# Optimization experiments

Hardware: AMD Instinct MI355X
Metric: run time of the kernel (lower is better)

The kernel has to match this reference:

```python
import jax, jax.numpy as jnp
import numpy as np

IN_C = 256
KEY_C = 256
VAL_C = 256
HEADS = 8


def setup_inputs() -> dict:
    key = jax.random.key(0)
    ks = jax.random.split(key, 9)
    s = 0.02
    return {
        "x": jax.random.normal(ks[0], (4, 8192, IN_C), dtype=jnp.float32),
        "Wk": jax.random.normal(ks[1], (KEY_C, IN_C), dtype=jnp.float32) * s,
        "bk": jax.random.normal(ks[2], (KEY_C,), dtype=jnp.float32) * s,
        "Wq": jax.random.normal(ks[3], (KEY_C, IN_C), dtype=jnp.float32) * s,
        "bq": jax.random.normal(ks[4], (KEY_C,), dtype=jnp.float32) * s,
        "Wv": jax.random.normal(ks[5], (VAL_C, IN_C), dtype=jnp.float32) * s,
        "bv": jax.random.normal(ks[6], (VAL_C,), dtype=jnp.float32) * s,
        "Wr": jax.random.normal(ks[7], (IN_C, VAL_C), dtype=jnp.float32) * s,
        "br": jax.random.normal(ks[8], (IN_C,), dtype=jnp.float32) * s,
    }


def reference(x, Wk, bk, Wq, bq, Wv, bv, Wr, br):
    n, N, c = x.shape
    # Faithful to torch: reshape (NOT transpose) of (n, N, c) into (n, c, N)
    xi = x.reshape(n, c, N)
    # 1x1 convs == channel-mixing matmuls over the token axis
    K = jnp.einsum('oc,ncs->nos', Wk, xi) + bk[None, :, None]
    Q = jnp.einsum('oc,ncs->nos', Wq, xi) + bq[None, :, None]
    V = jnp.einsum('oc,ncs->nos', Wv, xi) + bv[None, :, None]
    dk = KEY_C // HEADS
    dv = VAL_C // HEADS
    Kh = K.reshape(n, HEADS, dk, N)
    Qh = Q.reshape(n, HEADS, dk, N)
    Vh = V.reshape(n, HEADS, dv, N)
    # keys: softmax over tokens (dim=2); queries: softmax over head key channels (dim=1)
    Kh = jax.nn.softmax(Kh, axis=3)
    Qh = jax.nn.softmax(Qh, axis=2)
    # context = K @ V^T : [n, H, dk, dv]
    ctx = jnp.einsum('nhks,nhvs->nhkv', Kh, Vh)
    # attended = context^T @ Q : [n, H, dv, N]
    att = jnp.einsum('nhkv,nhks->nhvs', ctx, Qh)
    agg = att.reshape(n, VAL_C, N)
    rep = jnp.einsum('ov,nvs->nos', Wr, agg) + br[None, :, None]
    out = rep + xi  # residual in (n, c, N) layout
    return jnp.transpose(out, (0, 2, 1))  # (n, N, c)
```

## Files before the change

### kernel.cpp

```cpp
#include <hip/hip_runtime.h>

#define NTOK 8192
#define NCH  256
#define TT   64
#define XTP  264
#define EKP  72

typedef unsigned short u16;
typedef __attribute__((ext_vector_type(8))) short bf16x8;
typedef __attribute__((ext_vector_type(4))) float f32x4;
typedef __attribute__((ext_vector_type(8))) unsigned short u16x8;
typedef __attribute__((ext_vector_type(4))) unsigned short u16x4;

__device__ __forceinline__ float b2f(u16 h){
  union{unsigned u; float f;} x; x.u = ((unsigned)h) << 16; return x.f;
}
__device__ __forceinline__ u16 f2b(float f){
  union{float f; unsigned u;} x; x.f = f;
  unsigned u = x.u;
  return (u16)((u + 0x7FFFu + ((u >> 16) & 1u)) >> 16);
}
__device__ __forceinline__ f32x4 mfma16(bf16x8 a, bf16x8 b, f32x4 c){
  return __builtin_amdgcn_mfma_f32_16x16x32_bf16(a, b, c, 0, 0, 0);
}

__device__ __forceinline__ void stage_xtile(const float* __restrict__ xb,
                                            u16* scratch, u16* dst, int t)
{
  #pragma unroll
  for (int i = 0; i < 4; ++i) {
    int ch = i * 64 + (t >> 3);
    int tk = (t & 7) * 8;
    const float* p = xb + (size_t)ch * NTOK + tk;
    float4 v0 = *(const float4*)p;
    float4 v1 = *(const float4*)(p + 4);
    u16x8 pk;
    pk[0]=f2b(v0.x); pk[1]=f2b(v0.y); pk[2]=f2b(v0.z); pk[3]=f2b(v0.w);
    pk[4]=f2b(v1.x); pk[5]=f2b(v1.y); pk[6]=f2b(v1.z); pk[7]=f2b(v1.w);
    *(u16x8*)&scratch[ch * EKP + tk] = pk;
  }
  __syncthreads();
  #pragma unroll
  for (int p = 0; p < 4; ++p) {
    int idx = p * 512 + t;
    int tok = idx & 63;
    int ch = (idx >> 6) * 8;
    u16x8 o;
    #pragma unroll
    for (int j = 0; j < 8; ++j) o[j] = scratch[(ch + j) * EKP + tok];
    *(u16x8*)&dst[tok * XTP + ch] = o;
  }
}

__global__ __launch_bounds__(256)
void k_prep(const float* __restrict__ Wk, const float* __restrict__ Wq,
            const float* __restrict__ Wv, const float* __restrict__ Wr,
            u16* __restrict__ wbf)
{
  const int t = threadIdx.x, bid = blockIdx.x;
  const int mat = bid >> 4;
  const float* src = (mat == 0) ? Wk : (mat == 1) ? Wq : (mat == 2) ? Wv : Wr;
  u16* dst = wbf + mat * 65536;
  const int base = (bid & 15) * 4096 + t * 16;
  #pragma unroll
  for (int i = 0; i < 4; ++i) {
    float4 v = *(const float4*)(src + base + i * 4);
    u16x4 pk; pk[0]=f2b(v.x); pk[1]=f2b(v.y); pk[2]=f2b(v.z); pk[3]=f2b(v.w);
    *(u16x4*)(dst + base + i * 4) = pk;
  }
}

__global__ __launch_bounds__(512, 4)
void k_ctx(const float* __restrict__ x, const u16* __restrict__ wbf,
           const float* __restrict__ bk, const float* __restrict__ bv,
           u16* __restrict__ ctxPart, float* __restrict__ denomPart)
{
  __shared__ u16 bufA[NCH * EKP];
  __shared__ u16 ekb[NCH * EKP];

  const int t = threadIdx.x;
  const int b = blockIdx.x >> 7, g = blockIdx.x & 127;
  const int w = t >> 6, lane = t & 63;
  const int l15 = lane & 15, quad = lane >> 4;
  const u16* Wkb = wbf;
  const u16* Wvb = wbf + 2 * 65536;

  stage_xtile(x + (size_t)b * NCH * NTOK + g * TT, ekb, bufA, t);
  __syncthreads();

  f32x4 acc[2][4];

  #pragma unroll
  for (int mi = 0; mi < 2; ++mi)
    #pragma unroll
    for (int nj = 0; nj < 4; ++nj) acc[mi][nj] = (f32x4)0.f;
  for (int k0 = 0; k0 < NCH; k0 += 32) {
    bf16x8 af[2], bx[4];
    #pragma unroll
    for (int mi = 0; mi < 2; ++mi)
      af[mi] = *(const bf16x8*)(Wkb + (size_t)(w * 32 + mi * 16 + l15) * NCH + k0 + quad * 8);
    #pragma unroll
    for (int nj = 0; nj < 4; ++nj)
      bx[nj] = *(const bf16x8*)&bufA[(nj * 16 + l15) * XTP + k0 + quad * 8];
    #pragma unroll
    for (int mi = 0; mi < 2; ++mi)
      #pragma unroll
      for (int nj = 0; nj < 4; ++nj) acc[mi][nj] = mfma16(af[mi], bx[nj], acc[mi][nj]);
  }
  #pragma unroll
  for (int mi = 0; mi < 2; ++mi) {
    float4 bb = *(const float4*)(bk + w * 32 + mi * 16 + quad * 4);
    #pragma unroll
    for (int nj = 0; nj < 4; ++nj) {
      int tok = nj * 16 + l15, chb = w * 32 + mi * 16 + quad * 4;
      ekb[(chb + 0) * EKP + tok] = f2b(__expf(acc[mi][nj][0] + bb.x));
      ekb[(chb + 1) * EKP + tok] = f2b(__expf(acc[mi][nj][1] + bb.y));
      ekb[(chb + 2) * EKP + tok] = f2b(__expf(acc[mi][nj][2] + bb.z));
      ekb[(chb + 3) * EKP + tok] = f2b(__expf(acc[mi][nj][3] + bb.w));
    }
  }

  #pragma unroll
  for (int mi = 0; mi < 2; ++mi)
    #pragma unroll
    for (int nj = 0; nj < 4; ++nj) acc[mi][nj] = (f32x4)0.f;
  for (int k0 = 0; k0 < NCH; k0 += 32) {
    bf16x8 af[2], bx[4];
    #pragma unroll
    for (int mi = 0; mi < 2; ++mi)
      af[mi] = *(const bf16x8*)(Wvb + (size_t)(w * 32 + mi * 16 + l15) * NCH + k0 + quad * 8);
    #pragma unroll
    for (int nj = 0; nj < 4; ++nj)
      bx[nj] = *(const bf16x8*)&bufA[(nj * 16 + l15) * XTP + k0 + quad * 8];
    #pragma unroll
    for (int mi = 0; mi < 2; ++mi)
      #pragma unroll
      for (int nj = 0; nj < 4; ++nj) acc[mi][nj] = mfma16(af[mi], bx[nj], acc[mi][nj]);
  }
  __syncthreads();
  #pragma unroll
  for (int mi = 0; mi < 2; ++mi) {
    float4 bb = *(const float4*)(bv + w * 32 + mi * 16 + quad * 4);
    #pragma unroll
    for (int nj = 0; nj < 4; ++nj) {
      int tok = nj * 16 + l15, chb = w * 32 + mi * 16 + quad * 4;
      bufA[(chb + 0) * EKP + tok] = f2b(acc[mi][nj][0] + bb.x);
      bufA[(chb + 1) * EKP + tok] = f2b(acc[mi][nj][1] + bb.y);
      bufA[(chb + 2) * EKP + tok] = f2b(acc[mi][nj][2] + bb.z);
      bufA[(chb + 3) * EKP + tok] = f2b(acc[mi][nj][3] + bb.w);
    }
  }
  __syncthreads();

  f32x4 cacc[2][2];
  #pragma unroll
  for (int mi = 0; mi < 2; ++mi)
    #pragma unroll
    for (int nj = 0; nj < 2; ++nj) cacc[mi][nj] = (f32x4)0.f;
  #pragma unroll
  for (int kc = 0; kc < 2; ++kc) {
    bf16x8 ae[2], bvv[2];
    #pragma unroll
    for (int mi = 0; mi < 2; ++mi)
      ae[mi] = *(const bf16x8*)&ekb[(w * 32 + mi * 16 + l15) * EKP + kc * 32 + quad * 8];
    #pragma unroll
    for (int nj = 0; nj < 2; ++nj)
      bvv[nj] = *(const bf16x8*)&bufA[(w * 32 + nj * 16 + l15) * EKP + kc * 32 + quad * 8];
    #pragma unroll
    for (int mi = 0; mi < 2; ++mi)
      #pragma unroll
      for (int nj = 0; nj < 2; ++nj)
        cacc[mi][nj] = mfma16(ae[mi], bvv[nj], cacc[mi][nj]);
  }
  float dsum = 0.f;
  if (t < 256) {
    #pragma unroll
    for (int s = 0; s < TT; s += 8) {
      u16x8 v = *(const u16x8*)&ekb[t * EKP + s];
      #pragma unroll
      for (int j = 0; j < 8; ++j) dsum += b2f(v[j]);
    }
  }

  u16* cp = ctxPart + ((size_t)(b * 128 + g) << 13);
  #pragma unroll
  for (int mi = 0; mi < 2; ++mi)
    #pragma unroll
    for (int nj = 0; nj < 2; ++nj)
      #pragma unroll
      for (int r = 0; r < 4; ++r) {
        int e = ((w * 32 + mi * 16 + quad * 4 + r) << 5) + nj * 16 + l15;
        cp[e] = f2b(cacc[mi][nj][r]);
      }
  if (t < 256)
    denomPart[(size_t)(b * 128 + g) * 256 + t] = dsum;
}

__global__ __launch_bounds__(256)
void k_red(const u16* __restrict__ ctxPart, const float* __restrict__ denomPart,
           u16* __restrict__ ctxT, float* __restrict__ rdenomF)
{
  int i = blockIdx.x * 256 + threadIdx.x;
  if (i < 32768) {
    int b = i >> 13, e = i & 8191;
    const u16* p = ctxPart + ((size_t)(b * 128) << 13) + e;
    float s0 = 0.f, s1 = 0.f, s2 = 0.f, s3 = 0.f;
    #pragma unroll 8
    for (int g = 0; g < 128; g += 4) {
      s0 += b2f(p[(size_t)(g + 0) << 13]);
      s1 += b2f(p[(size_t)(g + 1) << 13]);
      s2 += b2f(p[(size_t)(g + 2) << 13]);
      s3 += b2f(p[(size_t)(g + 3) << 13]);
    }
    float s = (s0 + s1) + (s2 + s3);
    int hh = e >> 10, kk = (e >> 5) & 31, vch = e & 31;
    ctxT[(((b * 8 + hh) * 32 + vch) << 5) + kk] = f2b(s);
  } else if (i < 33792) {
    int j = i - 32768, b = j >> 8, ch = j & 255;
    const float* p = denomPart + (size_t)(b * 128) * 256 + ch;
    float s = 0.f;
    #pragma unroll 8
    for (int g = 0; g < 128; ++g) s += p[(size_t)g << 8];
    rdenomF[j] = 1.0f / s;
  }
}

__global__ __launch_bounds__(512, 4)
void k_out(const float* __restrict__ x, const u16* __restrict__ wbf,
           const float* __restrict__ bq, const float* __restrict__ br,
           const u16* __restrict__ ctxT, const float* __restrict__ rdenomF,
           float* __restrict__ out)
{
  __shared__ u16 xs[TT * XTP];
  __shared__ u16 qs[NCH * EKP];

  const int t = threadIdx.x;
  const int b = blockIdx.x >> 7, g = blockIdx.x & 127;
  const int w = t >> 6, lane = t & 63;
  const int l15 = lane & 15, quad = lane >> 4;
  const u16* Wqb = wbf + 65536;
  const u16* Wrb = wbf + 3 * 65536;

  stage_xtile(x + (size_t)b * NCH * NTOK + g * TT, qs, xs, t);
  __syncthreads();

  bf16x8 ac[2];
  #pragma unroll
  for (int mi = 0; mi < 2; ++mi)
    ac[mi] = *(const bf16x8*)(ctxT + (((size_t)(b * 8 + w) * 32 + mi * 16 + l15) << 5) + quad * 8);

  f32x4 acc[2][4];
  #pragma unroll
  for (int mi = 0; mi < 2; ++mi)
    #pragma unroll
    for (int nj = 0; nj < 4; ++nj) acc[mi][nj] = (f32x4)0.f;
  for (int k0 = 0; k0 < NCH; k0 += 32) {
    bf16x8 af[2], bx[4];
    #pragma unroll
    for (int mi = 0; mi < 2; ++mi)
      af[mi] = *(const bf16x8*)(Wqb + (size_t)(w * 32 + mi * 16 + l15) * NCH + k0 + quad * 8);
    #pragma unroll
    for (int nj = 0; nj < 4; ++nj)
      bx[nj] = *(const bf16x8*)&xs[(nj * 16 + l15) * XTP + k0 + quad * 8];
    #pragma unroll
    for (int mi = 0; mi < 2; ++mi)
      #pragma unroll
      for (int nj = 0; nj < 4; ++nj) acc[mi][nj] = mfma16(af[mi], bx[nj], acc[mi][nj]);
  }
  #pragma unroll
  for (int mi = 0; mi < 2; ++mi) {
    float4 bb = *(const float4*)(bq + w * 32 + mi * 16 + quad * 4);
    #pragma unroll
    for (int nj = 0; nj < 4; ++nj) {
      acc[mi][nj][0] = __expf(acc[mi][nj][0] + bb.x);
      acc[mi][nj][1] = __expf(acc[mi][nj][1] + bb.y);
      acc[mi][nj][2] = __expf(acc[mi][nj][2] + bb.z);
      acc[mi][nj][3] = __expf(acc[mi][nj][3] + bb.w);
    }
  }
  float inv[4];
  #pragma unroll
  for (int nj = 0; nj < 4; ++nj) {
    float s = 0.f;
    #pragma unroll
    for (int mi = 0; mi < 2; ++mi)
      #pragma unroll
      for (int r = 0; r < 4; ++r) s += acc[mi][nj][r];
    s += __shfl_xor(s, 16);
    s += __shfl_xor(s, 32);
    inv[nj] = 1.0f / s;
  }
  #pragma unroll
  for (int mi = 0; mi < 2; ++mi) {
    float4 rd = *(const float4*)(rdenomF + b * 256 + w * 32 + mi * 16 + quad * 4);
    #pragma unroll
    for (int nj = 0; nj < 4; ++nj) {
      u16x4 pk;
      pk[0] = f2b(acc[mi][nj][0] * inv[nj] * rd.x);
      pk[1] = f2b(acc[mi][nj][1] * inv[nj] * rd.y);
      pk[2] = f2b(acc[mi][nj][2] * inv[nj] * rd.z);
      pk[3] = f2b(acc[mi][nj][3] * inv[nj] * rd.w);
      *(u16x4*)&qs[(nj * 16 + l15) * XTP + w * 32 + mi * 16 + quad * 4] = pk;
    }
  }
  __syncthreads();

  f32x4 aacc[2][4];
  {
    #pragma unroll
    for (int nj = 0; nj < 4; ++nj) {
      bf16x8 bqf = *(const bf16x8*)&qs[(nj * 16 + l15) * XTP + w * 32 + quad * 8];
      #pragma unroll
      for (int mi = 0; mi < 2; ++mi)
        aacc[mi][nj] = mfma16(ac[mi], bqf, (f32x4)0.f);
    }
  }
  #pragma unroll
  for (int mi = 0; mi < 2; ++mi)
    #pragma unroll
    for (int nj = 0; nj < 4; ++nj) {
      u16x4 pk;
      pk[0] = f2b(aacc[mi][nj][0]);
      pk[1] = f2b(aacc[mi][nj][1]);
      pk[2] = f2b(aacc[mi][nj][2]);
      pk[3] = f2b(aacc[mi][nj][3]);
      *(u16x4*)&qs[(nj * 16 + l15) * XTP + w * 32 + mi * 16 + quad * 4] = pk;
    }
  __syncthreads();

  #pragma unroll
  for (int mi = 0; mi < 2; ++mi)
    #pragma unroll
    for (int nj = 0; nj < 4; ++nj) acc[mi][nj] = (f32x4)0.f;
  for (int k0 = 0; k0 < NCH; k0 += 32) {
    bf16x8 af[2], bx[4];
    #pragma unroll
    for (int mi = 0; mi < 2; ++mi)
      af[mi] = *(const bf16x8*)(Wrb + (size_t)(w * 32 + mi * 16 + l15) * NCH + k0 + quad * 8);
    #pragma unroll
    for (int nj = 0; nj < 4; ++nj)
      bx[nj] = *(const bf16x8*)&qs[(nj * 16 + l15) * XTP + k0 + quad * 8];
    #pragma unroll
    for (int mi = 0; mi < 2; ++mi)
      #pragma unroll
      for (int nj = 0; nj < 4; ++nj) acc[mi][nj] = mfma16(af[mi], bx[nj], acc[mi][nj]);
  }
  #pragma unroll
  for (int mi = 0; mi < 2; ++mi) {
    float4 bb = *(const float4*)(br + w * 32 + mi * 16 + quad * 4);
    #pragma unroll
    for (int nj = 0; nj < 4; ++nj) {
      int tok = nj * 16 + l15;
      u16x4 rx = *(const u16x4*)&xs[tok * XTP + w * 32 + mi * 16 + quad * 4];
      float4 o;
      o.x = acc[mi][nj][0] + bb.x + b2f(rx[0]);
      o.y = acc[mi][nj][1] + bb.y + b2f(rx[1]);
      o.z = acc[mi][nj][2] + bb.z + b2f(rx[2]);
      o.w = acc[mi][nj][3] + bb.w + b2f(rx[3]);
      *(float4*)(out + (((size_t)(b * NTOK + g * TT + tok)) << 8) + w * 32 + mi * 16 + quad * 4) = o;
    }
  }
}

extern "C" void kernel_launch(void* const* d_in, const int* in_sizes, int n_in,
                              void* d_out, int out_size, void* d_ws, size_t ws_size,
                              hipStream_t stream) {
  const float* x  = (const float*)d_in[0];
  const float* Wk = (const float*)d_in[1];
  const float* bk = (const float*)d_in[2];
  const float* Wq = (const float*)d_in[3];
  const float* bq = (const float*)d_in[4];
  const float* Wv = (const float*)d_in[5];
  const float* bv = (const float*)d_in[6];
  const float* Wr = (const float*)d_in[7];
  const float* br = (const float*)d_in[8];
  float* out = (float*)d_out;

  char* wsb = (char*)d_ws;
  u16*   ctxPart   = (u16*)wsb;
  float* denomPart = (float*)(wsb + 8388608);
  u16*   ctxT      = (u16*)(wsb + 8912896);
  float* rdenomF   = (float*)(wsb + 8978432);
  u16*   wbf       = (u16*)(wsb + 8982528);

  hipLaunchKernelGGL(k_prep, dim3(64), dim3(256), 0, stream,
                     Wk, Wq, Wv, Wr, wbf);
  hipLaunchKernelGGL(k_ctx, dim3(512), dim3(512), 0, stream,
                     x, wbf, bk, bv, ctxPart, denomPart);
  hipLaunchKernelGGL(k_red, dim3(132), dim3(256), 0, stream,
                     ctxPart, denomPart, ctxT, rdenomF);
  hipLaunchKernelGGL(k_out, dim3(512), dim3(512), 0, stream,
                     x, wbf, bq, br, ctxT, rdenomF, out);
}
```

Before: 144.9 us.

## Fuse context, reduction and output kernels into one persistent kernel with grid barriers

Merges k_ctx, k_red and k_out into a single kernel that keeps each block's x tile in LDS and syncs the whole grid twice through atomic counters. The counters are reset in k_prep. Q projection, softmax and the residual x values are computed and held in registers before the barrier, so x is not re-read and re-staged and there are fewer launches. The risks are the spin-wait barrier cost, higher register pressure from holding qacc and rx across the barriers, and deadlock if all 512 blocks are not co-resident.

```diff
diff --git a/kernel.cpp b/kernel.cpp
--- a/kernel.cpp
+++ b/kernel.cpp
@@ -5,6 +5,7 @@
 #define TT   64
 #define XTP  264
 #define EKP  72
+#define NBLK 512
 
 typedef unsigned short u16;
 typedef __attribute__((ext_vector_type(8))) short bf16x8;
@@ -22,6 +23,18 @@
 }
 __device__ __forceinline__ f32x4 mfma16(bf16x8 a, bf16x8 b, f32x4 c){
   return __builtin_amdgcn_mfma_f32_16x16x32_bf16(a, b, c, 0, 0, 0);
+}
+
+__device__ __forceinline__ void grid_sync(unsigned* cnt, int t) {
+  __syncthreads();
+  if (t == 0) {
+    __threadfence();
+    __hip_atomic_fetch_add(cnt, 1u, __ATOMIC_ACQ_REL, __HIP_MEMORY_SCOPE_AGENT);
+    while (__hip_atomic_load(cnt, __ATOMIC_ACQUIRE, __HIP_MEMORY_SCOPE_AGENT) < NBLK)
+      __builtin_amdgcn_s_sleep(1);
+    __threadfence();
+  }
+  __syncthreads();
 }
 
 __device__ __forceinline__ void stage_xtile(const float* __restrict__ xb,
@@ -55,9 +68,10 @@
 __global__ __launch_bounds__(256)
 void k_prep(const float* __restrict__ Wk, const float* __restrict__ Wq,
             const float* __restrict__ Wv, const float* __restrict__ Wr,
-            u16* __restrict__ wbf)
+            u16* __restrict__ wbf, unsigned* __restrict__ cnt)
 {
   const int t = threadIdx.x, bid = blockIdx.x;
+  if (bid == 0 && t == 0) { cnt[0] = 0u; cnt[1] = 0u; }
   const int mat = bid >> 4;
   const float* src = (mat == 0) ? Wk : (mat == 1) ? Wq : (mat == 2) ? Wv : Wr;
   u16* dst = wbf + mat * 65536;
@@ -71,9 +85,12 @@
 }
 
 __global__ __launch_bounds__(512, 4)
-void k_ctx(const float* __restrict__ x, const u16* __restrict__ wbf,
-           const float* __restrict__ bk, const float* __restrict__ bv,
-           u16* __restrict__ ctxPart, float* __restrict__ denomPart)
+void k_main(const float* __restrict__ x, const u16* __restrict__ wbf,
+            const float* __restrict__ bk, const float* __restrict__ bv,
+            const float* __restrict__ bq, const float* __restrict__ br,
+            u16* __restrict__ ctxPart, float* __restrict__ denomPart,
+            u16* __restrict__ ctxT, float* __restrict__ rdenomF,
+            float* __restrict__ out, unsigned* __restrict__ cnt)
 {
   __shared__ u16 bufA[NCH * EKP];
   __shared__ u16 ekb[NCH * EKP];
@@ -83,7 +100,9 @@
   const int w = t >> 6, lane = t & 63;
   const int l15 = lane & 15, quad = lane >> 4;
   const u16* Wkb = wbf;
+  const u16* Wqb = wbf + 65536;
   const u16* Wvb = wbf + 2 * 65536;
+  const u16* Wrb = wbf + 3 * 65536;
 
   stage_xtile(x + (size_t)b * NCH * NTOK + g * TT, ekb, bufA, t);
   __syncthreads();
@@ -120,6 +139,54 @@
     }
   }
 
+  f32x4 qacc[2][4];
+  #pragma unroll
+  for (int mi = 0; mi < 2; ++mi)
+    #pragma unroll
+    for (int nj = 0; nj < 4; ++nj) qacc[mi][nj] = (f32x4)0.f;
+  for (int k0 = 0; k0 < NCH; k0 += 32) {
+    bf16x8 af[2], bx[4];
+    #pragma unroll
+    for (int mi = 0; mi < 2; ++mi)
+      af[mi] = *(const bf16x8*)(Wqb + (size_t)(w * 32 + mi * 16 + l15) * NCH + k0 + quad * 8);
+    #pragma unroll
+    for (int nj = 0; nj < 4; ++nj)
+      bx[nj] = *(const bf16x8*)&bufA[(nj * 16 + l15) * XTP + k0 + quad * 8];
+    #pragma unroll
+    for (int mi = 0; mi < 2; ++mi)
+      #pragma unroll
+      for (int nj = 0; nj < 4; ++nj) qacc[mi][nj] = mfma16(af[mi], bx[nj], qacc[mi][nj]);
+  }
+  #pragma unroll
+  for (int mi = 0; mi < 2; ++mi) {
+    float4 bb = *(const float4*)(bq + w * 32 + mi * 16 + quad * 4);
+    #pragma unroll
+    for (int nj = 0; nj < 4; ++nj) {
+      qacc[mi][nj][0] = __expf(qacc[mi][nj][0] + bb.x);
+      qacc[mi][nj][1] = __expf(qacc[mi][nj][1] + bb.y);
+      qacc[mi][nj][2] = __expf(qacc[mi][nj][2] + bb.z);
+      qacc[mi][nj][3] = __expf(qacc[mi][nj][3] + bb.w);
+    }
+  }
+  float inv[4];
+  #pragma unroll
+  for (int nj = 0; nj < 4; ++nj) {
+    float s = 0.f;
+    #pragma unroll
+    for (int mi = 0; mi < 2; ++mi)
+      #pragma unroll
+      for (int r = 0; r < 4; ++r) s += qacc[mi][nj][r];
+    s += __shfl_xor(s, 16);
+    s += __shfl_xor(s, 32);
+    inv[nj] = 1.0f / s;
+  }
+  u16x4 rx[2][4];
+  #pragma unroll
+  for (int mi = 0; mi < 2; ++mi)
+    #pragma unroll
+    for (int nj = 0; nj < 4; ++nj)
+      rx[mi][nj] = *(const u16x4*)&bufA[(nj * 16 + l15) * XTP + w * 32 + mi * 16 + quad * 4];
+
   #pragma unroll
   for (int mi = 0; mi < 2; ++mi)
     #pragma unroll
@@ -182,124 +249,68 @@
     }
   }
 
-  u16* cp = ctxPart + ((size_t)(b * 128 + g) << 13);
-  #pragma unroll
-  for (int mi = 0; mi < 2; ++mi)
-    #pragma unroll
-    for (int nj = 0; nj < 2; ++nj)
-      #pragma unroll
-      for (int r = 0; r < 4; ++r) {
-        int e = ((w * 32 + mi * 16 + quad * 4 + r) << 5) + nj * 16 + l15;
-        cp[e] = f2b(cacc[mi][nj][r]);
+  {
+    u16* cp = ctxPart + ((size_t)(b * 128 + g) << 13);
+    #pragma unroll
+    for (int mi = 0; mi < 2; ++mi)
+      #pragma unroll
+      for (int nj = 0; nj < 2; ++nj)
+        #pragma unroll
+        for (int r = 0; r < 4; ++r) {
+          int e = ((w * 32 + mi * 16 + quad * 4 + r) << 5) + nj * 16 + l15;
+          cp[e] = f2b(cacc[mi][nj][r]);
+        }
+    if (t < 256)
+      denomPart[(size_t)(b * 128 + g) * 256 + t] = dsum;
+  }
+
+  grid_sync(&cnt[0], t);
+
+  {
+    const int gid = blockIdx.x * 512 + t;
+    if (gid < 32768) {
+      const int b2 = gid >> 13, e = gid & 8191;
+      const u16* p = ctxPart + (((size_t)b2 * 128) << 13) + e;
+      float s0 = 0.f, s1 = 0.f, s2 = 0.f, s3 = 0.f;
+      #pragma unroll 8
+      for (int g2 = 0; g2 < 128; g2 += 4) {
+        s0 += b2f(p[(size_t)(g2 + 0) << 13]);
+        s1 += b2f(p[(size_t)(g2 + 1) << 13]);
+        s2 += b2f(p[(size_t)(g2 + 2) << 13]);
+        s3 += b2f(p[(size_t)(g2 + 3) << 13]);
       }
-  if (t < 256)
-    denomPart[(size_t)(b * 128 + g) * 256 + t] = dsum;
-}
-
-__global__ __launch_bounds__(256)
-void k_red(const u16* __restrict__ ctxPart, const float* __restrict__ denomPart,
-           u16* __restrict__ ctxT, float* __restrict__ rdenomF)
-{
-  int i = blockIdx.x * 256 + threadIdx.x;
-  if (i < 32768) {
-    int b = i >> 13, e = i & 8191;
-    const u16* p = ctxPart + ((size_t)(b * 128) << 13) + e;
-    float s0 = 0.f, s1 = 0.f, s2 = 0.f, s3 = 0.f;
-    #pragma unroll 8
-    for (int g = 0; g < 128; g += 4) {
-      s0 += b2f(p[(size_t)(g + 0) << 13]);
-      s1 += b2f(p[(size_t)(g + 1) << 13]);
-      s2 += b2f(p[(size_t)(g + 2) << 13]);
-      s3 += b2f(p[(size_t)(g + 3) << 13]);
-    }
-    float s = (s0 + s1) + (s2 + s3);
-    int hh = e >> 10, kk = (e >> 5) & 31, vch = e & 31;
-    ctxT[(((b * 8 + hh) * 32 + vch) << 5) + kk] = f2b(s);
-  } else if (i < 33792) {
-    int j = i - 32768, b = j >> 8, ch = j & 255;
-    const float* p = denomPart + (size_t)(b * 128) * 256 + ch;
-    float s = 0.f;
-    #pragma unroll 8
-    for (int g = 0; g < 128; ++g) s += p[(size_t)g << 8];
-    rdenomF[j] = 1.0f / s;
-  }
-}
-
-__global__ __launch_bounds__(512, 4)
-void k_out(const float* __restrict__ x, const u16* __restrict__ wbf,
-           const float* __restrict__ bq, const float* __restrict__ br,
-           const u16* __restrict__ ctxT, const float* __restrict__ rdenomF,
-           float* __restrict__ out)
-{
-  __shared__ u16 xs[TT * XTP];
-  __shared__ u16 qs[NCH * EKP];
-
-  const int t = threadIdx.x;
-  const int b = blockIdx.x >> 7, g = blockIdx.x & 127;
-  const int w = t >> 6, lane = t & 63;
-  const int l15 = lane & 15, quad = lane >> 4;
-  const u16* Wqb = wbf + 65536;
-  const u16* Wrb = wbf + 3 * 65536;
-
-  stage_xtile(x + (size_t)b * NCH * NTOK + g * TT, qs, xs, t);
-  __syncthreads();
+      float s = (s0 + s1) + (s2 + s3);
+      int hh = e >> 10, kk = (e >> 5) & 31, vch = e & 31;
+      ctxT[(((b2 * 8 + hh) * 32 + vch) << 5) + kk] = f2b(s);
+    } else if (gid < 33792) {
+      int j = gid - 32768, b2 = j >> 8, ch = j & 255;
+      const float* p = denomPart + (size_t)(b2 * 128) * 256 + ch;
+      float s = 0.f;
+      #pragma unroll 8
+      for (int g2 = 0; g2 < 128; ++g2) s += p[(size_t)g2 << 8];
+      rdenomF[j] = 1.0f / s;
+    }
+  }
+
+  grid_sync(&cnt[1], t);
+
+  u16* qs = ekb;
 
   bf16x8 ac[2];
   #pragma unroll
   for (int mi = 0; mi < 2; ++mi)
     ac[mi] = *(const bf16x8*)(ctxT + (((size_t)(b * 8 + w) * 32 + mi * 16 + l15) << 5) + quad * 8);
 
-  f32x4 acc[2][4];
-  #pragma unroll
-  for (int mi = 0; mi < 2; ++mi)
-    #pragma unroll
-    for (int nj = 0; nj < 4; ++nj) acc[mi][nj] = (f32x4)0.f;
-  for (int k0 = 0; k0 < NCH; k0 += 32) {
-    bf16x8 af[2], bx[4];
-    #pragma unroll
-    for (int mi = 0; mi < 2; ++mi)
-      af[mi] = *(const bf16x8*)(Wqb + (size_t)(w * 32 + mi * 16 + l15) * NCH + k0 + quad * 8);
-    #pragma unroll
-    for (int nj = 0; nj < 4; ++nj)
-      bx[nj] = *(const bf16x8*)&xs[(nj * 16 + l15) * XTP + k0 + quad * 8];
-    #pragma unroll
-    for (int mi = 0; mi < 2; ++mi)
-      #pragma unroll
-      for (int nj = 0; nj < 4; ++nj) acc[mi][nj] = mfma16(af[mi], bx[nj], acc[mi][nj]);
-  }
-  #pragma unroll
-  for (int mi = 0; mi < 2; ++mi) {
-    float4 bb = *(const float4*)(bq + w * 32 + mi * 16 + quad * 4);
-    #pragma unroll
-    for (int nj = 0; nj < 4; ++nj) {
-      acc[mi][nj][0] = __expf(acc[mi][nj][0] + bb.x);
-      acc[mi][nj][1] = __expf(acc[mi][nj][1] + bb.y);
-      acc[mi][nj][2] = __expf(acc[mi][nj][2] + bb.z);
-      acc[mi][nj][3] = __expf(acc[mi][nj][3] + bb.w);
-    }
-  }
-  float inv[4];
-  #pragma unroll
-  for (int nj = 0; nj < 4; ++nj) {
-    float s = 0.f;
-    #pragma unroll
-    for (int mi = 0; mi < 2; ++mi)
-      #pragma unroll
-      for (int r = 0; r < 4; ++r) s += acc[mi][nj][r];
-    s += __shfl_xor(s, 16);
-    s += __shfl_xor(s, 32);
-    inv[nj] = 1.0f / s;
-  }
   #pragma unroll
   for (int mi = 0; mi < 2; ++mi) {
     float4 rd = *(const float4*)(rdenomF + b * 256 + w * 32 + mi * 16 + quad * 4);
     #pragma unroll
     for (int nj = 0; nj < 4; ++nj) {
       u16x4 pk;
-      pk[0] = f2b(acc[mi][nj][0] * inv[nj] * rd.x);
-      pk[1] = f2b(acc[mi][nj][1] * inv[nj] * rd.y);
-      pk[2] = f2b(acc[mi][nj][2] * inv[nj] * rd.z);
-      pk[3] = f2b(acc[mi][nj][3] * inv[nj] * rd.w);
+      pk[0] = f2b(qacc[mi][nj][0] * inv[nj] * rd.x);
+      pk[1] = f2b(qacc[mi][nj][1] * inv[nj] * rd.y);
+      pk[2] = f2b(qacc[mi][nj][2] * inv[nj] * rd.z);
+      pk[3] = f2b(qacc[mi][nj][3] * inv[nj] * rd.w);
       *(u16x4*)&qs[(nj * 16 + l15) * XTP + w * 32 + mi * 16 + quad * 4] = pk;
     }
   }
@@ -351,12 +362,11 @@
     #pragma unroll
     for (int nj = 0; nj < 4; ++nj) {
       int tok = nj * 16 + l15;
-      u16x4 rx = *(const u16x4*)&xs[tok * XTP + w * 32 + mi * 16 + quad * 4];
       float4 o;
-      o.x = acc[mi][nj][0] + bb.x + b2f(rx[0]);
-      o.y = acc[mi][nj][1] + bb.y + b2f(rx[1]);
-      o.z = acc[mi][nj][2] + bb.z + b2f(rx[2]);
-      o.w = acc[mi][nj][3] + bb.w + b2f(rx[3]);
+      o.x = acc[mi][nj][0] + bb.x + b2f(rx[mi][nj][0]);
+      o.y = acc[mi][nj][1] + bb.y + b2f(rx[mi][nj][1]);
+      o.z = acc[mi][nj][2] + bb.z + b2f(rx[mi][nj][2]);
+      o.w = acc[mi][nj][3] + bb.w + b2f(rx[mi][nj][3]);
       *(float4*)(out + (((size_t)(b * NTOK + g * TT + tok)) << 8) + w * 32 + mi * 16 + quad * 4) = o;
     }
   }
@@ -377,18 +387,16 @@
   float* out = (float*)d_out;
 
   char* wsb = (char*)d_ws;
-  u16*   ctxPart   = (u16*)wsb;
-  float* denomPart = (float*)(wsb + 8388608);
-  u16*   ctxT      = (u16*)(wsb + 8912896);
-  float* rdenomF   = (float*)(wsb + 8978432);
-  u16*   wbf       = (u16*)(wsb + 8982528);
+  u16*      ctxPart   = (u16*)wsb;
+  float*    denomPart = (float*)(wsb + 8388608);
+  u16*      ctxT      = (u16*)(wsb + 8912896);
+  float*    rdenomF   = (float*)(wsb + 8978432);
+  u16*      wbf       = (u16*)(wsb + 8982528);
+  unsigned* cnt       = (unsigned*)(wsb + 9506816);
 
   hipLaunchKernelGGL(k_prep, dim3(64), dim3(256), 0, stream,
-                     Wk, Wq, Wv, Wr, wbf);
-  hipLaunchKernelGGL(k_ctx, dim3(512), dim3(512), 0, stream,
-                     x, wbf, bk, bv, ctxPart, denomPart);
-  hipLaunchKernelGGL(k_red, dim3(132), dim3(256), 0, stream,
-                     ctxPart, denomPart, ctxT, rdenomF);
-  hipLaunchKernelGGL(k_out, dim3(512), dim3(512), 0, stream,
-                     x, wbf, bq, br, ctxT, rdenomF, out);
-}
+                     Wk, Wq, Wv, Wr, wbf, cnt);
+  hipLaunchKernelGGL(k_main, dim3(NBLK), dim3(512), 0, stream,
+                     x, wbf, bk, bv, bq, br,
+                     ctxPart, denomPart, ctxT, rdenomF, out, cnt);
+}
```

New measurement: 319.5 us. 2.2x slower.

## Cache bf16 transposed x tile from k_ctx for k_out; vectorize ctx reduction

Applied to the files above, without the earlier changes.

k_ctx now writes its staged bf16 token-major x tile to a workspace buffer. k_out reads that buffer directly instead of re-reading fp32 x and re-running the transpose and conversion in stage_xtile, which halves k_out's input traffic. The ctx partial reduction now has each thread sum 8 contiguous elements with 16-byte loads, which cuts the grid to 20 blocks. The cost is an extra bf16 write of x from k_ctx, and the small reduction grid may leave most of the GPU idle.

```diff
diff --git a/kernel.cpp b/kernel.cpp
--- a/kernel.cpp
+++ b/kernel.cpp
@@ -73,6 +73,7 @@
 __global__ __launch_bounds__(512, 4)
 void k_ctx(const float* __restrict__ x, const u16* __restrict__ wbf,
            const float* __restrict__ bk, const float* __restrict__ bv,
+           u16* __restrict__ xT,
            u16* __restrict__ ctxPart, float* __restrict__ denomPart)
 {
   __shared__ u16 bufA[NCH * EKP];
@@ -88,6 +89,16 @@
   stage_xtile(x + (size_t)b * NCH * NTOK + g * TT, ekb, bufA, t);
   __syncthreads();
 
+  {
+    u16* dst = xT + ((size_t)(b * NTOK + g * TT) << 8);
+    #pragma unroll
+    for (int i = 0; i < 4; ++i) {
+      int f = i * 4096 + t * 8;
+      int tok = f >> 8, ch = f & 255;
+      *(u16x8*)(dst + f) = *(const u16x8*)&bufA[tok * XTP + ch];
+    }
+  }
+
   f32x4 acc[2][4];
 
   #pragma unroll
@@ -201,22 +212,25 @@
            u16* __restrict__ ctxT, float* __restrict__ rdenomF)
 {
   int i = blockIdx.x * 256 + threadIdx.x;
-  if (i < 32768) {
-    int b = i >> 13, e = i & 8191;
-    const u16* p = ctxPart + ((size_t)(b * 128) << 13) + e;
-    float s0 = 0.f, s1 = 0.f, s2 = 0.f, s3 = 0.f;
-    #pragma unroll 8
-    for (int g = 0; g < 128; g += 4) {
-      s0 += b2f(p[(size_t)(g + 0) << 13]);
-      s1 += b2f(p[(size_t)(g + 1) << 13]);
-      s2 += b2f(p[(size_t)(g + 2) << 13]);
-      s3 += b2f(p[(size_t)(g + 3) << 13]);
-    }
-    float s = (s0 + s1) + (s2 + s3);
-    int hh = e >> 10, kk = (e >> 5) & 31, vch = e & 31;
-    ctxT[(((b * 8 + hh) * 32 + vch) << 5) + kk] = f2b(s);
-  } else if (i < 33792) {
-    int j = i - 32768, b = j >> 8, ch = j & 255;
+  if (i < 4096) {
+    const int base = i * 8;
+    const int b = base >> 13, e = base & 8191;
+    const u16* p = ctxPart + (((size_t)b * 128) << 13) + e;
+    float s[8];
+    #pragma unroll
+    for (int j = 0; j < 8; ++j) s[j] = 0.f;
+    #pragma unroll 4
+    for (int g = 0; g < 128; ++g) {
+      u16x8 v = *(const u16x8*)(p + ((size_t)g << 13));
+      #pragma unroll
+      for (int j = 0; j < 8; ++j) s[j] += b2f(v[j]);
+    }
+    const int hh = e >> 10, kk = (e >> 5) & 31, vchb = e & 31;
+    #pragma unroll
+    for (int j = 0; j < 8; ++j)
+      ctxT[(((b * 8 + hh) * 32 + vchb + j) << 5) + kk] = f2b(s[j]);
+  } else if (i < 5120) {
+    int j = i - 4096, b = j >> 8, ch = j & 255;
     const float* p = denomPart + (size_t)(b * 128) * 256 + ch;
     float s = 0.f;
     #pragma unroll 8
@@ -226,13 +240,13 @@
 }
 
 __global__ __launch_bounds__(512, 4)
-void k_out(const float* __restrict__ x, const u16* __restrict__ wbf,
+void k_out(const u16* __restrict__ xT, const u16* __restrict__ wbf,
            const float* __restrict__ bq, const float* __restrict__ br,
            const u16* __restrict__ ctxT, const float* __restrict__ rdenomF,
            float* __restrict__ out)
 {
   __shared__ u16 xs[TT * XTP];
-  __shared__ u16 qs[NCH * EKP];
+  __shared__ u16 qs[TT * XTP];
 
   const int t = threadIdx.x;
   const int b = blockIdx.x >> 7, g = blockIdx.x & 127;
@@ -241,7 +255,15 @@
   const u16* Wqb = wbf + 65536;
   const u16* Wrb = wbf + 3 * 65536;
 
-  stage_xtile(x + (size_t)b * NCH * NTOK + g * TT, qs, xs, t);
+  {
+    const u16* src = xT + ((size_t)(b * NTOK + g * TT) << 8);
+    #pragma unroll
+    for (int i = 0; i < 4; ++i) {
+      int f = i * 4096 + t * 8;
+      int tok = f >> 8, ch = f & 255;
+      *(u16x8*)&xs[tok * XTP + ch] = *(const u16x8*)(src + f);
+    }
+  }
   __syncthreads();
 
   bf16x8 ac[2];
@@ -382,13 +404,14 @@
   u16*   ctxT      = (u16*)(wsb + 8912896);
   float* rdenomF   = (float*)(wsb + 8978432);
   u16*   wbf       = (u16*)(wsb + 8982528);
+  u16*   xT        = (u16*)(wsb + 9506816);
 
   hipLaunchKernelGGL(k_prep, dim3(64), dim3(256), 0, stream,
                      Wk, Wq, Wv, Wr, wbf);
   hipLaunchKernelGGL(k_ctx, dim3(512), dim3(512), 0, stream,
-                     x, wbf, bk, bv, ctxPart, denomPart);
-  hipLaunchKernelGGL(k_red, dim3(132), dim3(256), 0, stream,
+                     x, wbf, bk, bv, xT, ctxPart, denomPart);
+  hipLaunchKernelGGL(k_red, dim3(20), dim3(256), 0, stream,
                      ctxPart, denomPart, ctxT, rdenomF);
   hipLaunchKernelGGL(k_out, dim3(512), dim3(512), 0, stream,
-                     x, wbf, bq, br, ctxT, rdenomF, out);
-}
+                     xT, wbf, bq, br, ctxT, rdenomF, out);
+}
```

Measured after the change: 154.5 us. 6.6% more time.

## Compute normalized Q in k_ctx and stream it to k_out via workspace

Applied to the files above, without the earlier changes.

The Q projection and its per-token softmax move from k_out into k_ctx, which already holds the staged x tile, and normalized Q is written to a global bf16 buffer. k_out then loads that precomputed Q tile instead of re-staging x and running a GEMM. It reads the fp32 residual directly from x, and folds the key denominators into the ctx fragment instead of scaling Q. This avoids staging x twice and halves k_out's shared memory, but adds a 16 MB bf16 write and read of Q and uncoalesced strided residual loads.

```diff
diff --git a/kernel.cpp b/kernel.cpp
--- a/kernel.cpp
+++ b/kernel.cpp
@@ -72,7 +72,9 @@
 
 __global__ __launch_bounds__(512, 4)
 void k_ctx(const float* __restrict__ x, const u16* __restrict__ wbf,
-           const float* __restrict__ bk, const float* __restrict__ bv,
+           const float* __restrict__ bk, const float* __restrict__ bq,
+           const float* __restrict__ bv,
+           u16* __restrict__ qnG,
            u16* __restrict__ ctxPart, float* __restrict__ denomPart)
 {
   __shared__ u16 bufA[NCH * EKP];
@@ -83,6 +85,7 @@
   const int w = t >> 6, lane = t & 63;
   const int l15 = lane & 15, quad = lane >> 4;
   const u16* Wkb = wbf;
+  const u16* Wqb = wbf + 65536;
   const u16* Wvb = wbf + 2 * 65536;
 
   stage_xtile(x + (size_t)b * NCH * NTOK + g * TT, ekb, bufA, t);
@@ -118,6 +121,61 @@
       ekb[(chb + 2) * EKP + tok] = f2b(__expf(acc[mi][nj][2] + bb.z));
       ekb[(chb + 3) * EKP + tok] = f2b(__expf(acc[mi][nj][3] + bb.w));
     }
+  }
+
+  #pragma unroll
+  for (int mi = 0; mi < 2; ++mi)
+    #pragma unroll
+    for (int nj = 0; nj < 4; ++nj) acc[mi][nj] = (f32x4)0.f;
+  for (int k0 = 0; k0 < NCH; k0 += 32) {
+    bf16x8 af[2], bx[4];
+    #pragma unroll
+    for (int mi = 0; mi < 2; ++mi)
+      af[mi] = *(const bf16x8*)(Wqb + (size_t)(w * 32 + mi * 16 + l15) * NCH + k0 + quad * 8);
+    #pragma unroll
+    for (int nj = 0; nj < 4; ++nj)
+      bx[nj] = *(const bf16x8*)&bufA[(nj * 16 + l15) * XTP + k0 + quad * 8];
+    #pragma unroll
+    for (int mi = 0; mi < 2; ++mi)
+      #pragma unroll
+      for (int nj = 0; nj < 4; ++nj) acc[mi][nj] = mfma16(af[mi], bx[nj], acc[mi][nj]);
+  }
+  {
+    #pragma unroll
+    for (int mi = 0; mi < 2; ++mi) {
+      float4 bb = *(const float4*)(bq + w * 32 + mi * 16 + quad * 4);
+      #pragma unroll
+      for (int nj = 0; nj < 4; ++nj) {
+        acc[mi][nj][0] = __expf(acc[mi][nj][0] + bb.x);
+        acc[mi][nj][1] = __expf(acc[mi][nj][1] + bb.y);
+        acc[mi][nj][2] = __expf(acc[mi][nj][2] + bb.z);
+        acc[mi][nj][3] = __expf(acc[mi][nj][3] + bb.w);
+      }
+    }
+    float inv[4];
+    #pragma unroll
+    for (int nj = 0; nj < 4; ++nj) {
+      float s = 0.f;
+      #pragma unroll
+      for (int mi = 0; mi < 2; ++mi)
+        #pragma unroll
+        for (int r = 0; r < 4; ++r) s += acc[mi][nj][r];
+      s += __shfl_xor(s, 16);
+      s += __shfl_xor(s, 32);
+      inv[nj] = 1.0f / s;
+    }
+    u16* qdst = qnG + ((size_t)(b * 128 + g) << 14);
+    #pragma unroll
+    for (int mi = 0; mi < 2; ++mi)
+      #pragma unroll
+      for (int nj = 0; nj < 4; ++nj) {
+        u16x4 pk;
+        pk[0] = f2b(acc[mi][nj][0] * inv[nj]);
+        pk[1] = f2b(acc[mi][nj][1] * inv[nj]);
+        pk[2] = f2b(acc[mi][nj][2] * inv[nj]);
+        pk[3] = f2b(acc[mi][nj][3] * inv[nj]);
+        *(u16x4*)(qdst + ((nj * 16 + l15) << 8) + w * 32 + mi * 16 + quad * 4) = pk;
+      }
   }
 
   #pragma unroll
@@ -227,80 +285,51 @@
 
 __global__ __launch_bounds__(512, 4)
 void k_out(const float* __restrict__ x, const u16* __restrict__ wbf,
-           const float* __restrict__ bq, const float* __restrict__ br,
+           const float* __restrict__ br,
            const u16* __restrict__ ctxT, const float* __restrict__ rdenomF,
-           float* __restrict__ out)
+           const u16* __restrict__ qnG, float* __restrict__ out)
 {
-  __shared__ u16 xs[TT * XTP];
-  __shared__ u16 qs[NCH * EKP];
+  __shared__ u16 qs[TT * XTP];
 
   const int t = threadIdx.x;
   const int b = blockIdx.x >> 7, g = blockIdx.x & 127;
   const int w = t >> 6, lane = t & 63;
   const int l15 = lane & 15, quad = lane >> 4;
-  const u16* Wqb = wbf + 65536;
   const u16* Wrb = wbf + 3 * 65536;
 
-  stage_xtile(x + (size_t)b * NCH * NTOK + g * TT, qs, xs, t);
-  __syncthreads();
+  {
+    const u16* src = qnG + ((size_t)(b * 128 + g) << 14);
+    #pragma unroll
+    for (int i = 0; i < 4; ++i) {
+      int f = i * 4096 + t * 8;
+      int tok = f >> 8, ch = f & 255;
+      *(u16x8*)&qs[tok * XTP + ch] = *(const u16x8*)(src + f);
+    }
+  }
+
+  float resv[2][4][4];
+  {
+    const float* xr = x + (size_t)b * NCH * NTOK + g * TT;
+    #pragma unroll
+    for (int mi = 0; mi < 2; ++mi)
+      #pragma unroll
+      for (int nj = 0; nj < 4; ++nj)
+        #pragma unroll
+        for (int r = 0; r < 4; ++r)
+          resv[mi][nj][r] = xr[(size_t)(w * 32 + mi * 16 + quad * 4 + r) * NTOK + nj * 16 + l15];
+  }
 
   bf16x8 ac[2];
-  #pragma unroll
-  for (int mi = 0; mi < 2; ++mi)
-    ac[mi] = *(const bf16x8*)(ctxT + (((size_t)(b * 8 + w) * 32 + mi * 16 + l15) << 5) + quad * 8);
-
-  f32x4 acc[2][4];
-  #pragma unroll
-  for (int mi = 0; mi < 2; ++mi)
-    #pragma unroll
-    for (int nj = 0; nj < 4; ++nj) acc[mi][nj] = (f32x4)0.f;
-  for (int k0 = 0; k0 < NCH; k0 += 32) {
-    bf16x8 af[2], bx[4];
-    #pragma unroll
-    for (int mi = 0; mi < 2; ++mi)
-      af[mi] = *(const bf16x8*)(Wqb + (size_t)(w * 32 + mi * 16 + l15) * NCH + k0 + quad * 8);
-    #pragma unroll
-    for (int nj = 0; nj < 4; ++nj)
-      bx[nj] = *(const bf16x8*)&xs[(nj * 16 + l15) * XTP + k0 + quad * 8];
-    #pragma unroll
-    for (int mi = 0; mi < 2; ++mi)
-      #pragma unroll
-      for (int nj = 0; nj < 4; ++nj) acc[mi][nj] = mfma16(af[mi], bx[nj], acc[mi][nj]);
-  }
-  #pragma unroll
-  for (int mi = 0; mi < 2; ++mi) {
-    float4 bb = *(const float4*)(bq + w * 32 + mi * 16 + quad * 4);
-    #pragma unroll
-    for (int nj = 0; nj < 4; ++nj) {
-      acc[mi][nj][0] = __expf(acc[mi][nj][0] + bb.x);
-      acc[mi][nj][1] = __expf(acc[mi][nj][1] + bb.y);
-      acc[mi][nj][2] = __expf(acc[mi][nj][2] + bb.z);
-      acc[mi][nj][3] = __expf(acc[mi][nj][3] + bb.w);
-    }
-  }
-  float inv[4];
-  #pragma unroll
-  for (int nj = 0; nj < 4; ++nj) {
-    float s = 0.f;
-    #pragma unroll
-    for (int mi = 0; mi < 2; ++mi)
-      #pragma unroll
-      for (int r = 0; r < 4; ++r) s += acc[mi][nj][r];
-    s += __shfl_xor(s, 16);
-    s += __shfl_xor(s, 32);
-    inv[nj] = 1.0f / s;
-  }
-  #pragma unroll
-  for (int mi = 0; mi < 2; ++mi) {
-    float4 rd = *(const float4*)(rdenomF + b * 256 + w * 32 + mi * 16 + quad * 4);
-    #pragma unroll
-    for (int nj = 0; nj < 4; ++nj) {
-      u16x4 pk;
-      pk[0] = f2b(acc[mi][nj][0] * inv[nj] * rd.x);
-      pk[1] = f2b(acc[mi][nj][1] * inv[nj] * rd.y);
-      pk[2] = f2b(acc[mi][nj][2] * inv[nj] * rd.z);
-      pk[3] = f2b(acc[mi][nj][3] * inv[nj] * rd.w);
-      *(u16x4*)&qs[(nj * 16 + l15) * XTP + w * 32 + mi * 16 + quad * 4] = pk;
+  {
+    float4 r0 = *(const float4*)(rdenomF + b * 256 + w * 32 + quad * 8);
+    float4 r1 = *(const float4*)(rdenomF + b * 256 + w * 32 + quad * 8 + 4);
+    float rd[8] = {r0.x, r0.y, r0.z, r0.w, r1.x, r1.y, r1.z, r1.w};
+    #pragma unroll
+    for (int mi = 0; mi < 2; ++mi) {
+      bf16x8 c = *(const bf16x8*)(ctxT + (((size_t)(b * 8 + w) * 32 + mi * 16 + l15) << 5) + quad * 8);
+      #pragma unroll
+      for (int j = 0; j < 8; ++j)
+        ac[mi][j] = (short)f2b(b2f((u16)c[j]) * rd[j]);
     }
   }
   __syncthreads();
@@ -328,6 +357,7 @@
     }
   __syncthreads();
 
+  f32x4 acc[2][4];
   #pragma unroll
   for (int mi = 0; mi < 2; ++mi)
     #pragma unroll
@@ -351,12 +381,11 @@
     #pragma unroll
     for (int nj = 0; nj < 4; ++nj) {
       int tok = nj * 16 + l15;
-      u16x4 rx = *(const u16x4*)&xs[tok * XTP + w * 32 + mi * 16 + quad * 4];
       float4 o;
-      o.x = acc[mi][nj][0] + bb.x + b2f(rx[0]);
-      o.y = acc[mi][nj][1] + bb.y + b2f(rx[1]);
-      o.z = acc[mi][nj][2] + bb.z + b2f(rx[2]);
-      o.w = acc[mi][nj][3] + bb.w + b2f(rx[3]);
+      o.x = acc[mi][nj][0] + bb.x + resv[mi][nj][0];
+      o.y = acc[mi][nj][1] + bb.y + resv[mi][nj][1];
+      o.z = acc[mi][nj][2] + bb.z + resv[mi][nj][2];
+      o.w = acc[mi][nj][3] + bb.w + resv[mi][nj][3];
       *(float4*)(out + (((size_t)(b * NTOK + g * TT + tok)) << 8) + w * 32 + mi * 16 + quad * 4) = o;
     }
   }
@@ -382,13 +411,14 @@
   u16*   ctxT      = (u16*)(wsb + 8912896);
   float* rdenomF   = (float*)(wsb + 8978432);
   u16*   wbf       = (u16*)(wsb + 8982528);
+  u16*   qnG       = (u16*)(wsb + 9506816);
 
   hipLaunchKernelGGL(k_prep, dim3(64), dim3(256), 0, stream,
                      Wk, Wq, Wv, Wr, wbf);
   hipLaunchKernelGGL(k_ctx, dim3(512), dim3(512), 0, stream,
-                     x, wbf, bk, bv, ctxPart, denomPart);
+                     x, wbf, bk, bq, bv, qnG, ctxPart, denomPart);
   hipLaunchKernelGGL(k_red, dim3(132), dim3(256), 0, stream,
                      ctxPart, denomPart, ctxT, rdenomF);
   hipLaunchKernelGGL(k_out, dim3(512), dim3(512), 0, stream,
-                     x, wbf, bq, br, ctxT, rdenomF, out);
-}
+                     x, wbf, br, ctxT, rdenomF, qnG, out);
+}
```

After: 148.3 us. +2.3%, slower.
